# Kernel optimization log

Hardware: AMD Instinct MI355X
Metric: run time of the kernel (lower is better)

Reference implementation:

```python
import jax, jax.numpy as jnp
import numpy as np

IN_F, OUT_F = 4096, 11008
MAXQ = 15  # 2**4 - 1 for wbits=4


def setup_inputs() -> dict:
    key = jax.random.key(0)
    k1, k2, k3, k4, k5 = jax.random.split(key, 5)
    inp = jax.random.normal(k1, (4, 64, IN_F), dtype=jnp.float32)
    weight = jax.random.normal(k2, (OUT_F, IN_F), dtype=jnp.float32) * 0.02
    bias = jax.random.normal(k3, (OUT_F,), dtype=jnp.float32) * 0.02
    # per-channel asymmetric quant params (as Quantizer.find_params would produce)
    scale = jax.random.uniform(k4, (OUT_F, 1), dtype=jnp.float32) * 0.01 + 1e-4
    zero = jnp.round(jax.random.uniform(k5, (OUT_F, 1), dtype=jnp.float32) * MAXQ)
    return {"input": inp, "weight": weight, "bias": bias,
            "scale": scale, "zero": zero, "maxq": MAXQ}


def reference(input, weight, bias, scale, zero, maxq):
    # fake-quantize weight: q = clamp(round(w/scale) + zero, 0, maxq); w_dq = scale*(q - zero)
    q = jnp.clip(jnp.round(weight / scale) + zero, 0.0, float(maxq))
    w_dq = scale * (q - zero)                      # [out, in]
    # F.linear: input @ w_dq.T + bias
    out = jnp.einsum('bsi,oi->bso', input, w_dq) + bias
    return out
```

## Files before the change

kernel.cpp:

```cpp
#include <hip/hip_runtime.h>
#include <hip/hip_bf16.h>
#include <stdint.h>

#define K_TOT 4096
#define N_TOT 11008
#define M_TOT 256
#define BM 128
#define BN 64
#define WST 72

using bf16x8 = __attribute__((ext_vector_type(8))) short;
using f32x4  = __attribute__((ext_vector_type(4))) float;

__global__ void cvt_a_bf16(const float* __restrict__ in, uint32_t* __restrict__ out) {
    int i = blockIdx.x * blockDim.x + threadIdx.x;
    const float4 v = ((const float4*)in)[i];
    uint32_t a = __float_as_uint(v.x), b = __float_as_uint(v.y),
             c = __float_as_uint(v.z), d = __float_as_uint(v.w);
    a += 0x7FFFu + ((a >> 16) & 1u);
    b += 0x7FFFu + ((b >> 16) & 1u);
    c += 0x7FFFu + ((c >> 16) & 1u);
    d += 0x7FFFu + ((d >> 16) & 1u);
    uint2 o;
    o.x = (a >> 16) | (b & 0xFFFF0000u);
    o.y = (c >> 16) | (d & 0xFFFF0000u);
    ((uint2*)out)[i] = o;
}

__device__ __forceinline__ void dequant16(const float4 w[4], float rs, float zp, float sc,
                                          uint32_t o[8]) {
    float f[16];
#pragma unroll
    for (int j = 0; j < 4; ++j) {
        f[4 * j + 0] = w[j].x; f[4 * j + 1] = w[j].y;
        f[4 * j + 2] = w[j].z; f[4 * j + 3] = w[j].w;
    }
    uint32_t u[16];
#pragma unroll
    for (int i = 0; i < 16; ++i) {
        float q = rintf(f[i] * rs) + zp;
        q = fminf(fmaxf(q, 0.0f), 15.0f);
        float dq = (q - zp) * sc;
        uint32_t b = __float_as_uint(dq);
        u[i] = b + 0x7FFFu + ((b >> 16) & 1u);
    }
#pragma unroll
    for (int i = 0; i < 8; ++i)
        o[i] = (u[2 * i] >> 16) | (u[2 * i + 1] & 0xFFFF0000u);
}

__device__ __forceinline__ void compute_step(f32x4 acc[4][2], const uint16_t* const Ap[4],
                                             const uint16_t (*sw)[WST], int kt, int wn, int lane) {
    const int koff = kt * 64;
#pragma unroll
    for (int s = 0; s < 2; ++s) {
        bf16x8 a[4], b[2];
#pragma unroll
        for (int mi = 0; mi < 4; ++mi)
            a[mi] = *(const bf16x8*)(Ap[mi] + koff + s * 32);
#pragma unroll
        for (int ni = 0; ni < 2; ++ni)
            b[ni] = *(const bf16x8*)&sw[wn + ni * 16 + (lane & 15)][s * 32 + (lane >> 4) * 8];
#pragma unroll
        for (int mi = 0; mi < 4; ++mi)
#pragma unroll
            for (int ni = 0; ni < 2; ++ni)
                acc[mi][ni] = __builtin_amdgcn_mfma_f32_16x16x32_bf16(a[mi], b[ni], acc[mi][ni], 0, 0, 0);
    }
}

__global__ __launch_bounds__(256, 4)
void wql_gemm(const uint16_t* __restrict__ A,
              const float* __restrict__ W,
              const float* __restrict__ scale,
              const float* __restrict__ zero,
              float* __restrict__ P,
              int kloc) {
    __shared__ uint16_t sW[2][BN][WST];

    const int tid  = threadIdx.x;
    const int lane = tid & 63;
    const int wv   = tid >> 6;
    const int wm   = (wv & 1) * 64;
    const int wn   = (wv >> 1) * 32;
    const int m0   = blockIdx.x * BM;
    const int n0   = blockIdx.y * BN;
    const int k0   = blockIdx.z * kloc;
    const int nkt  = kloc / 64;

    const int nloc = tid >> 2;
    const int kseg = tid & 3;
    const int wrow = n0 + nloc;
    const float* Wp = W + (size_t)wrow * K_TOT + k0 + kseg * 16;
    const float sc = scale[wrow];
    const float zp = zero[wrow];
    const float rs = 1.0f / sc;
    uint16_t* sdst0 = &sW[0][nloc][kseg * 16];
    uint16_t* sdst1 = &sW[1][nloc][kseg * 16];

    const uint16_t* Ap[4];
#pragma unroll
    for (int mi = 0; mi < 4; ++mi)
        Ap[mi] = A + (size_t)(m0 + wm + mi * 16 + (lane & 15)) * K_TOT + k0 + (lane >> 4) * 8;

    f32x4 acc[4][2];
#pragma unroll
    for (int mi = 0; mi < 4; ++mi)
#pragma unroll
        for (int ni = 0; ni < 2; ++ni)
            acc[mi][ni] = (f32x4){0.f, 0.f, 0.f, 0.f};

    float4 bank0[4], bank1[4];

#pragma unroll
    for (int j = 0; j < 4; ++j) bank0[j] = ((const float4*)Wp)[j];
    {
        uint32_t o[8];
        dequant16(bank0, rs, zp, sc, o);
        ((uint4*)sdst0)[0] = make_uint4(o[0], o[1], o[2], o[3]);
        ((uint4*)sdst0)[1] = make_uint4(o[4], o[5], o[6], o[7]);
    }
#pragma unroll
    for (int j = 0; j < 4; ++j) bank1[j] = ((const float4*)(Wp + 64))[j];
    __syncthreads();

    for (int kt = 0; kt < nkt; kt += 2) {
        if (kt + 2 < nkt) {
            const float4* p = (const float4*)(Wp + (size_t)(kt + 2) * 64);
#pragma unroll
            for (int j = 0; j < 4; ++j) bank0[j] = p[j];
        }
        compute_step(acc, Ap, sW[0], kt, wn, lane);
        {
            uint32_t o[8];
            dequant16(bank1, rs, zp, sc, o);
            ((uint4*)sdst1)[0] = make_uint4(o[0], o[1], o[2], o[3]);
            ((uint4*)sdst1)[1] = make_uint4(o[4], o[5], o[6], o[7]);
        }
        __syncthreads();

        if (kt + 3 < nkt) {
            const float4* p = (const float4*)(Wp + (size_t)(kt + 3) * 64);
#pragma unroll
            for (int j = 0; j < 4; ++j) bank1[j] = p[j];
        }
        compute_step(acc, Ap, sW[1], kt + 1, wn, lane);
        if (kt + 2 < nkt) {
            uint32_t o[8];
            dequant16(bank0, rs, zp, sc, o);
            ((uint4*)sdst0)[0] = make_uint4(o[0], o[1], o[2], o[3]);
            ((uint4*)sdst0)[1] = make_uint4(o[4], o[5], o[6], o[7]);
        }
        __syncthreads();
    }

    float* Pb = P + (size_t)blockIdx.z * M_TOT * N_TOT;
    const int colbase = n0 + wn + (lane & 15);
    const int rbase = m0 + wm + ((lane >> 4) << 2);
#pragma unroll
    for (int mi = 0; mi < 4; ++mi) {
#pragma unroll
        for (int ni = 0; ni < 2; ++ni) {
            const int col = colbase + ni * 16;
#pragma unroll
            for (int r = 0; r < 4; ++r) {
                const int row = rbase + mi * 16 + r;
                Pb[(size_t)row * N_TOT + col] = acc[mi][ni][r];
            }
        }
    }
}

__global__ void reduce_bias(const float* __restrict__ P, const float* __restrict__ bias,
                            float* __restrict__ out, int ks) {
    const int i4 = blockIdx.x * blockDim.x + threadIdx.x;
    const size_t tot4 = (size_t)M_TOT * N_TOT / 4;
    const int col = (int)(((size_t)i4 * 4) % N_TOT);
    float4 acc = ((const float4*)P)[i4];
    for (int s = 1; s < ks; ++s) {
        const float4 v = ((const float4*)P)[(size_t)s * tot4 + i4];
        acc.x += v.x; acc.y += v.y; acc.z += v.z; acc.w += v.w;
    }
    const float4 b = *(const float4*)(bias + col);
    acc.x += b.x; acc.y += b.y; acc.z += b.z; acc.w += b.w;
    ((float4*)out)[i4] = acc;
}

extern "C" void kernel_launch(void* const* d_in, const int* in_sizes, int n_in,
                              void* d_out, int out_size, void* d_ws, size_t ws_size,
                              hipStream_t stream) {
    const float* inp    = (const float*)d_in[0];
    const float* weight = (const float*)d_in[1];
    const float* bias   = (const float*)d_in[2];
    const float* scale  = (const float*)d_in[3];
    const float* zero   = (const float*)d_in[4];

    const size_t A_BYTES = (size_t)M_TOT * K_TOT * 2;
    const size_t SLICE   = (size_t)M_TOT * N_TOT * 4;

    uint32_t* Abf = (uint32_t*)d_ws;
    float* partial;
    int KS;
    if (ws_size >= A_BYTES + 4 * SLICE) { KS = 4; partial = (float*)((char*)d_ws + A_BYTES); }
    else if (ws_size >= A_BYTES + 2 * SLICE) { KS = 2; partial = (float*)((char*)d_ws + A_BYTES); }
    else { KS = 1; partial = (float*)d_out; }

    cvt_a_bf16<<<dim3((M_TOT * K_TOT / 4) / 256), dim3(256), 0, stream>>>(inp, Abf);

    dim3 grid(M_TOT / BM, N_TOT / BN, KS);
    wql_gemm<<<grid, dim3(256), 0, stream>>>((const uint16_t*)Abf, weight, scale, zero,
                                             partial, K_TOT / KS);

    reduce_bias<<<dim3((M_TOT * N_TOT / 4) / 256), dim3(256), 0, stream>>>(
        partial, bias, (float*)d_out, KS);
}
```

Before: 368.8 us.

## Drop LDS staging: each wave dequantizes its own weight fragment in registers

Removes the shared-memory double buffer and __syncthreads for the dequantized weight tile. Each wave now owns 16 output columns across all 128 rows, loads its fp32 weight fragment directly into registers, dequantizes it there into the MFMA B operand, and issues 8 MFMAs per k-step. The K loop length becomes a compile-time template parameter. This cuts LDS traffic and barriers, but each wave now reads all 128 rows of A from global memory, so A reads per block double, and register use rises from the 8 A fragments.

```diff
diff --git a/kernel.cpp b/kernel.cpp
--- a/kernel.cpp
+++ b/kernel.cpp
@@ -5,9 +5,6 @@
 #define K_TOT 4096
 #define N_TOT 11008
 #define M_TOT 256
-#define BM 128
-#define BN 64
-#define WST 72
 
 using bf16x8 = __attribute__((ext_vector_type(8))) short;
 using f32x4  = __attribute__((ext_vector_type(4))) float;
@@ -27,147 +24,82 @@
     ((uint2*)out)[i] = o;
 }
 
-__device__ __forceinline__ void dequant16(const float4 w[4], float rs, float zp, float sc,
-                                          uint32_t o[8]) {
-    float f[16];
-#pragma unroll
-    for (int j = 0; j < 4; ++j) {
-        f[4 * j + 0] = w[j].x; f[4 * j + 1] = w[j].y;
-        f[4 * j + 2] = w[j].z; f[4 * j + 3] = w[j].w;
-    }
-    uint32_t u[16];
-#pragma unroll
-    for (int i = 0; i < 16; ++i) {
-        float q = rintf(f[i] * rs) + zp;
-        q = fminf(fmaxf(q, 0.0f), 15.0f);
-        float dq = (q - zp) * sc;
-        uint32_t b = __float_as_uint(dq);
-        u[i] = b + 0x7FFFu + ((b >> 16) & 1u);
-    }
-#pragma unroll
-    for (int i = 0; i < 8; ++i)
-        o[i] = (u[2 * i] >> 16) | (u[2 * i + 1] & 0xFFFF0000u);
-}
-
-__device__ __forceinline__ void compute_step(f32x4 acc[4][2], const uint16_t* const Ap[4],
-                                             const uint16_t (*sw)[WST], int kt, int wn, int lane) {
-    const int koff = kt * 64;
-#pragma unroll
-    for (int s = 0; s < 2; ++s) {
-        bf16x8 a[4], b[2];
-#pragma unroll
-        for (int mi = 0; mi < 4; ++mi)
-            a[mi] = *(const bf16x8*)(Ap[mi] + koff + s * 32);
-#pragma unroll
-        for (int ni = 0; ni < 2; ++ni)
-            b[ni] = *(const bf16x8*)&sw[wn + ni * 16 + (lane & 15)][s * 32 + (lane >> 4) * 8];
-#pragma unroll
-        for (int mi = 0; mi < 4; ++mi)
-#pragma unroll
-            for (int ni = 0; ni < 2; ++ni)
-                acc[mi][ni] = __builtin_amdgcn_mfma_f32_16x16x32_bf16(a[mi], b[ni], acc[mi][ni], 0, 0, 0);
-    }
-}
-
+template <int NKT>
 __global__ __launch_bounds__(256, 4)
 void wql_gemm(const uint16_t* __restrict__ A,
               const float* __restrict__ W,
               const float* __restrict__ scale,
               const float* __restrict__ zero,
-              float* __restrict__ P,
-              int kloc) {
-    __shared__ uint16_t sW[2][BN][WST];
+              float* __restrict__ P) {
+    const int tid   = threadIdx.x;
+    const int lane  = tid & 63;
+    const int wv    = tid >> 6;
+    const int col16 = lane & 15;
+    const int kq    = lane >> 4;
+    const int m0    = blockIdx.x * 128;
+    const int n0    = blockIdx.y * 64;
+    const int k0    = blockIdx.z * (NKT * 32);
 
-    const int tid  = threadIdx.x;
-    const int lane = tid & 63;
-    const int wv   = tid >> 6;
-    const int wm   = (wv & 1) * 64;
-    const int wn   = (wv >> 1) * 32;
-    const int m0   = blockIdx.x * BM;
-    const int n0   = blockIdx.y * BN;
-    const int k0   = blockIdx.z * kloc;
-    const int nkt  = kloc / 64;
+    const int n = n0 + wv * 16 + col16;
+    const float sc = scale[n];
+    const float zp = zero[n];
+    const float rs = 1.0f / sc;
+    const float lo = -zp, hi = 15.0f - zp;
+    const float* Bp = W + (size_t)n * K_TOT + k0 + kq * 8;
 
-    const int nloc = tid >> 2;
-    const int kseg = tid & 3;
-    const int wrow = n0 + nloc;
-    const float* Wp = W + (size_t)wrow * K_TOT + k0 + kseg * 16;
-    const float sc = scale[wrow];
-    const float zp = zero[wrow];
-    const float rs = 1.0f / sc;
-    uint16_t* sdst0 = &sW[0][nloc][kseg * 16];
-    uint16_t* sdst1 = &sW[1][nloc][kseg * 16];
+    const uint16_t* Ap[8];
+#pragma unroll
+    for (int mi = 0; mi < 8; ++mi)
+        Ap[mi] = A + (size_t)(m0 + mi * 16 + col16) * K_TOT + k0 + kq * 8;
 
-    const uint16_t* Ap[4];
+    f32x4 acc[8];
 #pragma unroll
-    for (int mi = 0; mi < 4; ++mi)
-        Ap[mi] = A + (size_t)(m0 + wm + mi * 16 + (lane & 15)) * K_TOT + k0 + (lane >> 4) * 8;
+    for (int mi = 0; mi < 8; ++mi) acc[mi] = (f32x4){0.f, 0.f, 0.f, 0.f};
 
-    f32x4 acc[4][2];
+    float4 bn0 = ((const float4*)Bp)[0];
+    float4 bn1 = ((const float4*)Bp)[1];
+
+#pragma unroll 2
+    for (int kt = 0; kt < NKT; ++kt) {
+        bf16x8 a[8];
 #pragma unroll
-    for (int mi = 0; mi < 4; ++mi)
+        for (int mi = 0; mi < 8; ++mi)
+            a[mi] = *(const bf16x8*)(Ap[mi] + kt * 32);
+
+        float4 bc0 = bn0, bc1 = bn1;
+        if (kt + 1 < NKT) {
+            bn0 = *(const float4*)(Bp + (size_t)(kt + 1) * 32);
+            bn1 = *(const float4*)(Bp + (size_t)(kt + 1) * 32 + 4);
+        }
+
+        float f[8] = {bc0.x, bc0.y, bc0.z, bc0.w, bc1.x, bc1.y, bc1.z, bc1.w};
+        uint32_t u[8];
 #pragma unroll
-        for (int ni = 0; ni < 2; ++ni)
-            acc[mi][ni] = (f32x4){0.f, 0.f, 0.f, 0.f};
-
-    float4 bank0[4], bank1[4];
+        for (int i = 0; i < 8; ++i) {
+            float r = rintf(f[i] * rs);
+            r = fminf(fmaxf(r, lo), hi);
+            const uint32_t b = __float_as_uint(r * sc);
+            u[i] = b + 0x7FFFu + ((b >> 16) & 1u);
+        }
+        uint32_t p[4];
+#pragma unroll
+        for (int i = 0; i < 4; ++i)
+            p[i] = (u[2 * i] >> 16) | (u[2 * i + 1] & 0xFFFF0000u);
+        const bf16x8 bf = *(const bf16x8*)p;
 
 #pragma unroll
-    for (int j = 0; j < 4; ++j) bank0[j] = ((const float4*)Wp)[j];
-    {
-        uint32_t o[8];
-        dequant16(bank0, rs, zp, sc, o);
-        ((uint4*)sdst0)[0] = make_uint4(o[0], o[1], o[2], o[3]);
-        ((uint4*)sdst0)[1] = make_uint4(o[4], o[5], o[6], o[7]);
-    }
-#pragma unroll
-    for (int j = 0; j < 4; ++j) bank1[j] = ((const float4*)(Wp + 64))[j];
-    __syncthreads();
-
-    for (int kt = 0; kt < nkt; kt += 2) {
-        if (kt + 2 < nkt) {
-            const float4* p = (const float4*)(Wp + (size_t)(kt + 2) * 64);
-#pragma unroll
-            for (int j = 0; j < 4; ++j) bank0[j] = p[j];
-        }
-        compute_step(acc, Ap, sW[0], kt, wn, lane);
-        {
-            uint32_t o[8];
-            dequant16(bank1, rs, zp, sc, o);
-            ((uint4*)sdst1)[0] = make_uint4(o[0], o[1], o[2], o[3]);
-            ((uint4*)sdst1)[1] = make_uint4(o[4], o[5], o[6], o[7]);
-        }
-        __syncthreads();
-
-        if (kt + 3 < nkt) {
-            const float4* p = (const float4*)(Wp + (size_t)(kt + 3) * 64);
-#pragma unroll
-            for (int j = 0; j < 4; ++j) bank1[j] = p[j];
-        }
-        compute_step(acc, Ap, sW[1], kt + 1, wn, lane);
-        if (kt + 2 < nkt) {
-            uint32_t o[8];
-            dequant16(bank0, rs, zp, sc, o);
-            ((uint4*)sdst0)[0] = make_uint4(o[0], o[1], o[2], o[3]);
-            ((uint4*)sdst0)[1] = make_uint4(o[4], o[5], o[6], o[7]);
-        }
-        __syncthreads();
+        for (int mi = 0; mi < 8; ++mi)
+            acc[mi] = __builtin_amdgcn_mfma_f32_16x16x32_bf16(a[mi], bf, acc[mi], 0, 0, 0);
     }
 
     float* Pb = P + (size_t)blockIdx.z * M_TOT * N_TOT;
-    const int colbase = n0 + wn + (lane & 15);
-    const int rbase = m0 + wm + ((lane >> 4) << 2);
+    const int colg = n0 + wv * 16 + col16;
 #pragma unroll
-    for (int mi = 0; mi < 4; ++mi) {
+    for (int mi = 0; mi < 8; ++mi) {
+        const int rbase = m0 + mi * 16 + kq * 4;
 #pragma unroll
-        for (int ni = 0; ni < 2; ++ni) {
-            const int col = colbase + ni * 16;
-#pragma unroll
-            for (int r = 0; r < 4; ++r) {
-                const int row = rbase + mi * 16 + r;
-                Pb[(size_t)row * N_TOT + col] = acc[mi][ni][r];
-            }
-        }
+        for (int r = 0; r < 4; ++r)
+            Pb[(size_t)(rbase + r) * N_TOT + colg] = acc[mi][r];
     }
 }
 
@@ -199,18 +131,21 @@
     const size_t SLICE   = (size_t)M_TOT * N_TOT * 4;
 
     uint32_t* Abf = (uint32_t*)d_ws;
-    float* partial;
-    int KS;
-    if (ws_size >= A_BYTES + 4 * SLICE) { KS = 4; partial = (float*)((char*)d_ws + A_BYTES); }
-    else if (ws_size >= A_BYTES + 2 * SLICE) { KS = 2; partial = (float*)((char*)d_ws + A_BYTES); }
-    else { KS = 1; partial = (float*)d_out; }
 
     cvt_a_bf16<<<dim3((M_TOT * K_TOT / 4) / 256), dim3(256), 0, stream>>>(inp, Abf);
 
-    dim3 grid(M_TOT / BM, N_TOT / BN, KS);
-    wql_gemm<<<grid, dim3(256), 0, stream>>>((const uint16_t*)Abf, weight, scale, zero,
-                                             partial, K_TOT / KS);
-
-    reduce_bias<<<dim3((M_TOT * N_TOT / 4) / 256), dim3(256), 0, stream>>>(
-        partial, bias, (float*)d_out, KS);
+    if (ws_size >= A_BYTES + 4 * SLICE) {
+        float* partial = (float*)((char*)d_ws + A_BYTES);
+        dim3 grid(M_TOT / 128, N_TOT / 64, 4);
+        wql_gemm<32><<<grid, dim3(256), 0, stream>>>((const uint16_t*)Abf, weight,
+                                                     scale, zero, partial);
+        reduce_bias<<<dim3((M_TOT * N_TOT / 4) / 256), dim3(256), 0, stream>>>(
+            partial, bias, (float*)d_out, 4);
+    } else {
+        dim3 grid(M_TOT / 128, N_TOT / 64, 1);
+        wql_gemm<128><<<grid, dim3(256), 0, stream>>>((const uint16_t*)Abf, weight,
+                                                      scale, zero, (float*)d_out);
+        reduce_bias<<<dim3((M_TOT * N_TOT / 4) / 256), dim3(256), 0, stream>>>(
+            (float*)d_out, bias, (float*)d_out, 1);
+    }
 }
```

After: 448.9 us. 1.22x slower.
